# Kernel tuning notes

Measured on AMD Instinct MI355X. Metric: run time of the kernel, lower is better.

Reference implementation:

```python
import jax, jax.numpy as jnp
import numpy as np

B, N = 8192, 128          # batch, num intruders
D_OWN, D_GRID, D_INTR = 16, 512, 20
H, OUT = 128, 4


def setup_inputs() -> dict:
    key = jax.random.key(0)
    ks = jax.random.split(key, 12)
    rn = lambda k, shape, s=1.0: jax.random.normal(k, shape, jnp.float32) * s
    return {
        "state0": rn(ks[0], (B, D_OWN)),
        "state1": rn(ks[1], (B, D_GRID)),
        "state2": rn(ks[2], (B, N, D_INTR)),
        "W_own": rn(ks[3], (D_OWN, H), 0.1), "b_own": jnp.zeros((H,), jnp.float32),
        "W_intr": rn(ks[4], (D_INTR, H), 0.1), "b_intr": jnp.zeros((H,), jnp.float32),
        "W_grid": rn(ks[5], (D_GRID, H), 0.05), "b_grid": jnp.zeros((H,), jnp.float32),
        "Wq": rn(ks[6], (H, H), 0.08),
        "Wk": rn(ks[7], (H, H), 0.08),
        "Wv": rn(ks[8], (H, H), 0.08),
        "W1": rn(ks[9], (3 * H, H), 0.05), "b1": jnp.zeros((H,), jnp.float32),
        "W2": rn(ks[10], (H, OUT), 0.1), "b2": jnp.zeros((OUT,), jnp.float32),
    }


def reference(state0, state1, state2, W_own, b_own, W_intr, b_intr,
              W_grid, b_grid, Wq, Wk, Wv, W1, b1, W2, b2):
    own_e = jax.nn.relu(state0 @ W_own + b_own)            # [B,H]
    x_e = jax.nn.relu(state2 @ W_intr + b_intr)            # [B,N,H]
    q = own_e @ Wq                                         # [B,H]
    k = x_e @ Wk                                           # [B,N,H]
    v = x_e @ Wv                                           # [B,N,H]
    # mask = state2.mean(axis=2, keepdim=True).bool()  (nonzero test)
    mask = jnp.mean(state2, axis=2, keepdims=True) != 0    # [B,N,1]
    score = jnp.einsum('bnh,bh->bn', k, q)[..., None]      # bmm(k, q.unsqueeze(2)) -> [B,N,1]
    score = jnp.where(mask, score, -jnp.inf)
    alpha = jax.nn.softmax(score / np.float32(np.sqrt(H)), axis=1)
    alpha = jnp.where(mask, alpha, 0.0)
    v_att = jnp.sum(v * alpha, axis=1)                     # [B,H]
    own_grid = jax.nn.relu(state1 @ W_grid + b_grid)       # [B,H]
    concat = jnp.concatenate([own_e, v_att, own_grid], axis=1)  # [B,3H]
    out = (concat @ W1 + b1) @ W2 + b2                     # action_out_SAC
    mean = out
    log_std = jnp.clip(out, -20.0, 2.0)
    return mean, log_std
```

## Files before the change

### kernel.cpp

```cpp
#include <hip/hip_runtime.h>

typedef unsigned short ushort_t;
typedef __attribute__((ext_vector_type(8))) short bf16x8;
typedef __attribute__((ext_vector_type(4))) float f32x4;

__device__ __forceinline__ float bflo(unsigned u) { return __uint_as_float(u << 16); }
__device__ __forceinline__ float bfhi(unsigned u) { return __uint_as_float(u & 0xffff0000u); }
__device__ __forceinline__ float bfu(ushort_t s)  { return __uint_as_float((unsigned)s << 16); }
__device__ __forceinline__ ushort_t f2bf(float f) {
    unsigned u = __float_as_uint(f);
    u = u + 0x7fffu + ((u >> 16) & 1u);
    return (ushort_t)(u >> 16);
}
__device__ __forceinline__ void unpack8(uint4 v, float* f) {
    f[0]=bflo(v.x); f[1]=bfhi(v.x); f[2]=bflo(v.y); f[3]=bfhi(v.y);
    f[4]=bflo(v.z); f[5]=bfhi(v.z); f[6]=bflo(v.w); f[7]=bfhi(v.w);
}

__device__ __forceinline__ float load1(const void* p, size_t i, int f32) {
    return f32 ? ((const float*)p)[i] : bfu(((const ushort_t*)p)[i]);
}
__device__ __forceinline__ void load8(const void* p, size_t i, int f32, float* f) {
    if (f32) {
        const float4 a = *(const float4*)((const float*)p + i);
        const float4 b = *(const float4*)((const float*)p + i + 4);
        f[0]=a.x; f[1]=a.y; f[2]=a.z; f[3]=a.w;
        f[4]=b.x; f[5]=b.y; f[6]=b.z; f[7]=b.w;
    } else {
        unpack8(*(const uint4*)((const ushort_t*)p + i), f);
    }
}
__device__ __forceinline__ void load4(const void* p, size_t i, int f32, float* f) {
    if (f32) {
        const float4 a = *(const float4*)((const float*)p + i);
        f[0]=a.x; f[1]=a.y; f[2]=a.z; f[3]=a.w;
    } else {
        const uint2 u = *(const uint2*)((const ushort_t*)p + i);
        f[0]=bflo(u.x); f[1]=bfhi(u.x); f[2]=bflo(u.y); f[3]=bfhi(u.y);
    }
}

__device__ __forceinline__ int detect_f32(const ushort_t* s1h) {
    const int ln = threadIdx.x & 63;
    float v = fmaxf(fabsf(bfu(s1h[ln])), fabsf(bfu(s1h[ln + 64])));
    bool big = !(v <= 1e6f);
    return __ballot(big) != 0ull;
}

#define B_TOT 8192

__device__ __attribute__((aligned(16))) float    g_M[128 * 128];
__device__ __attribute__((aligned(16))) float    g_Wc1[384 * 4];
__device__ __attribute__((aligned(16))) float    g_Wv2[128 * 4];
__device__ __attribute__((aligned(16))) float    g_bc[4];
__device__ __attribute__((aligned(16))) float    g_t[B_TOT * 128];
__device__ __attribute__((aligned(16))) float    g_ogc[B_TOT * 4];
__device__ __attribute__((aligned(16))) ushort_t g_oe[B_TOT * 128];

__global__ __launch_bounds__(128) void k_pre(
    const void* __restrict__ Wq, const void* __restrict__ Wk,
    const void* __restrict__ Wv, const void* __restrict__ W1,
    const void* __restrict__ b1, const void* __restrict__ W2,
    const void* __restrict__ b2, const ushort_t* __restrict__ s1h)
{
    __shared__ float wq_sh[128];
    __shared__ float w2_sh[512];
    __shared__ float wc1_mid[512];
    __shared__ float redc[128][4];
    const int tid = threadIdx.x;
    const int bx = blockIdx.x;
    const int f32 = detect_f32(s1h);

    if (bx < 128) {
        wq_sh[tid] = load1(Wq, bx*128 + tid, f32);
        __syncthreads();
        float acc = 0.f;
        #pragma unroll
        for (int c = 0; c < 16; ++c) {
            float f[8]; load8(Wk, (size_t)tid*128 + c*8, f32, f);
            #pragma unroll
            for (int j = 0; j < 8; ++j) acc = fmaf(wq_sh[c*8+j], f[j], acc);
        }
        g_M[bx*128 + tid] = acc;
    } else {
        const int rbase = (bx == 128) ? 0 : ((bx == 129) ? 128 : 256);
        for (int i = tid; i < 512; i += 128) w2_sh[i] = load1(W2, i, f32);
        __syncthreads();

        const int r = rbase + tid;
        float a[4] = {0.f, 0.f, 0.f, 0.f};
        #pragma unroll
        for (int c = 0; c < 16; ++c) {
            float f[8]; load8(W1, (size_t)r*128 + c*8, f32, f);
            #pragma unroll
            for (int j = 0; j < 8; ++j) {
                const int p = c*8 + j;
                #pragma unroll
                for (int q = 0; q < 4; ++q) a[q] = fmaf(f[j], w2_sh[p*4+q], a[q]);
            }
        }
        #pragma unroll
        for (int q = 0; q < 4; ++q) g_Wc1[r*4+q] = a[q];

        if (bx == 129) {
            #pragma unroll
            for (int q = 0; q < 4; ++q) wc1_mid[tid*4+q] = a[q];
            __syncthreads();
            float v[4] = {0.f, 0.f, 0.f, 0.f};
            #pragma unroll
            for (int c = 0; c < 16; ++c) {
                float f[8]; load8(Wv, (size_t)tid*128 + c*8, f32, f);
                #pragma unroll
                for (int j = 0; j < 8; ++j) {
                    const int i2 = c*8 + j;
                    #pragma unroll
                    for (int q = 0; q < 4; ++q) v[q] = fmaf(f[j], wc1_mid[i2*4+q], v[q]);
                }
            }
            #pragma unroll
            for (int q = 0; q < 4; ++q) g_Wv2[tid*4+q] = v[q];

            const float bv = load1(b1, tid, f32);
            #pragma unroll
            for (int q = 0; q < 4; ++q) redc[tid][q] = bv * w2_sh[tid*4+q];
            __syncthreads();
            for (int s = 64; s > 0; s >>= 1) {
                if (tid < s) {
                    #pragma unroll
                    for (int q = 0; q < 4; ++q) redc[tid][q] += redc[tid+s][q];
                }
                __syncthreads();
            }
            if (tid < 4) g_bc[tid] = redc[0][tid] + load1(b2, tid, f32);
        }
    }
}

struct OwntSmem {
    float s0sh[16*16];
    float wosh[16*128];
    float bosh[128];
    float oesh[16*129];
    float Mt[32][128];
};
struct GridSmem {
    float s1T[32][18];
    float wg[32][128];
    float part[32][16][4];
};

__global__ __launch_bounds__(256) void k_og(
    const void* __restrict__ state0, const void* __restrict__ W_own,
    const void* __restrict__ b_own, const void* __restrict__ state1,
    const void* __restrict__ W_grid, const void* __restrict__ b_grid,
    const ushort_t* __restrict__ s1h)
{
    __shared__ __attribute__((aligned(16))) char smem_raw[
        sizeof(OwntSmem) > sizeof(GridSmem) ? sizeof(OwntSmem) : sizeof(GridSmem)];
    const int tid = threadIdx.x;
    const int bxx = blockIdx.x;
    const int f32 = detect_f32(s1h);

    if (bxx < 512) {
        OwntSmem& S = *reinterpret_cast<OwntSmem*>(smem_raw);
        const int b0 = bxx * 16;

        if (tid < 32) {
            float f[8]; load8(state0, (size_t)b0*16 + tid*8, f32, f);
            #pragma unroll
            for (int j = 0; j < 8; ++j) S.s0sh[tid*8 + j] = f[j];
        }
        {
            float f[8]; load8(W_own, (size_t)tid*8, f32, f);
            #pragma unroll
            for (int j = 0; j < 8; ++j) S.wosh[tid*8 + j] = f[j];
        }
        if (tid < 128) S.bosh[tid] = load1(b_own, tid, f32);
        __syncthreads();

        #pragma unroll
        for (int kk = 0; kk < 8; ++kk) {
            const int idx = tid + kk*256;
            const int bi = idx >> 7, h = idx & 127;
            float acc = S.bosh[h];
            #pragma unroll
            for (int d = 0; d < 16; ++d) acc = fmaf(S.s0sh[bi*16+d], S.wosh[d*128+h], acc);
            acc = fmaxf(acc, 0.f);
            S.oesh[bi*129 + h] = acc;
            g_oe[(size_t)(b0+bi)*128 + h] = f2bf(acc);
        }

        const int bi0 = (tid >> 5) * 2;
        const int h0  = (tid & 31) * 4;
        float t00=0.f,t01=0.f,t02=0.f,t03=0.f,t10=0.f,t11=0.f,t12=0.f,t13=0.f;
        for (int kt = 0; kt < 128; kt += 32) {
            __syncthreads();
            #pragma unroll
            for (int c = 0; c < 4; ++c) {
                const int i = tid + c*256;
                const int kk = i >> 5;
                const int hh = (i & 31) * 4;
                *(float4*)&S.Mt[kk][hh] = *(const float4*)&g_M[(size_t)(kt+kk)*128 + hh];
            }
            __syncthreads();
            #pragma unroll
            for (int k = 0; k < 32; ++k) {
                const float4 mv = *(const float4*)&S.Mt[k][h0];
                const float a0 = S.oesh[(bi0+0)*129 + kt + k];
                const float a1 = S.oesh[(bi0+1)*129 + kt + k];
                t00=fmaf(a0,mv.x,t00); t01=fmaf(a0,mv.y,t01); t02=fmaf(a0,mv.z,t02); t03=fmaf(a0,mv.w,t03);
                t10=fmaf(a1,mv.x,t10); t11=fmaf(a1,mv.y,t11); t12=fmaf(a1,mv.z,t12); t13=fmaf(a1,mv.w,t13);
            }
        }
        *(float4*)&g_t[(size_t)(b0+bi0+0)*128 + h0] = make_float4(t00,t01,t02,t03);
        *(float4*)&g_t[(size_t)(b0+bi0+1)*128 + h0] = make_float4(t10,t11,t12,t13);
    } else {
        GridSmem& S = *reinterpret_cast<GridSmem*>(smem_raw);
        const int b0 = (bxx - 512) * 16;

        const int bq = tid & 7;
        const int hq = tid >> 3;
        float a00=0.f,a01=0.f,a02=0.f,a03=0.f;
        float a10=0.f,a11=0.f,a12=0.f,a13=0.f;

        for (int kt = 0; kt < 512; kt += 32) {
            if (kt) __syncthreads();
            if (tid < 128) {
                const int bb = tid >> 3;
                const int kk = (tid & 7) * 4;
                float f[4];
                load4(state1, (size_t)(b0 + bb)*512 + kt + kk, f32, f);
                #pragma unroll
                for (int j = 0; j < 4; ++j) S.s1T[kk + j][bb] = f[j];
            }
            {
                #pragma unroll
                for (int c = 0; c < 4; ++c) {
                    const int i = tid + c*256;
                    const int kk = i >> 5;
                    const int hh = (i & 31) * 4;
                    float f[4];
                    load4(W_grid, (size_t)(kt + kk)*128 + hh, f32, f);
                    *(float4*)&S.wg[kk][hh] = make_float4(f[0], f[1], f[2], f[3]);
                }
            }
            __syncthreads();
            #pragma unroll 8
            for (int k = 0; k < 32; ++k) {
                const float x0 = S.s1T[k][bq*2 + 0];
                const float x1 = S.s1T[k][bq*2 + 1];
                const float4 w = *(const float4*)&S.wg[k][hq*4];
                a00=fmaf(x0,w.x,a00); a01=fmaf(x0,w.y,a01); a02=fmaf(x0,w.z,a02); a03=fmaf(x0,w.w,a03);
                a10=fmaf(x1,w.x,a10); a11=fmaf(x1,w.y,a11); a12=fmaf(x1,w.z,a12); a13=fmaf(x1,w.w,a13);
            }
        }

        float accs[2][4] = {{a00,a01,a02,a03},{a10,a11,a12,a13}};
        float pr[2][4] = {{0,0,0,0},{0,0,0,0}};
        #pragma unroll
        for (int jh = 0; jh < 4; ++jh) {
            const int h = hq*4 + jh;
            const float bg = load1(b_grid, h, f32);
            const float4 wc = *(const float4*)&g_Wc1[(256 + h)*4];
            #pragma unroll
            for (int ib = 0; ib < 2; ++ib) {
                const float og = fmaxf(accs[ib][jh] + bg, 0.f);
                pr[ib][0] = fmaf(og, wc.x, pr[ib][0]);
                pr[ib][1] = fmaf(og, wc.y, pr[ib][1]);
                pr[ib][2] = fmaf(og, wc.z, pr[ib][2]);
                pr[ib][3] = fmaf(og, wc.w, pr[ib][3]);
            }
        }
        __syncthreads();
        #pragma unroll
        for (int j = 0; j < 4; ++j) {
            S.part[hq][bq*2+0][j] = pr[0][j];
            S.part[hq][bq*2+1][j] = pr[1][j];
        }
        __syncthreads();
        if (tid < 64) {
            const int bb = tid >> 2, j = tid & 3;
            float s = 0.f;
            #pragma unroll
            for (int q = 0; q < 32; ++q) s += S.part[q][bb][j];
            g_ogc[(size_t)(b0 + bb)*4 + j] = s;
        }
    }
}

__global__ __launch_bounds__(256) void k_main(
    const void* __restrict__ state2, const void* __restrict__ W_intr,
    const void* __restrict__ b_intr, const ushort_t* __restrict__ s1h,
    void* __restrict__ out_raw)
{
    __shared__ __attribute__((aligned(16))) ushort_t wib[128 * 40];
    const int tid = threadIdx.x;
    const int f32 = detect_f32(s1h);

    #pragma unroll
    for (int c = 0; c < 10; ++c) {
        const int idx = c*256 + tid;
        const int d = idx >> 7, h = idx & 127;
        wib[h*40 + d] = f32 ? f2bf(((const float*)W_intr)[idx])
                            : ((const ushort_t*)W_intr)[idx];
    }
    if (tid < 128) {
        #pragma unroll
        for (int k = 20; k < 32; ++k) wib[tid*40 + k] = 0;
    }
    __syncthreads();

    const int wv = tid >> 6, ln = tid & 63, lq = ln >> 4, lc = ln & 15;
    const int b = blockIdx.x * 4 + wv;

    float bi_r[8], t_r[8];
    #pragma unroll
    for (int th = 0; th < 8; ++th) {
        bi_r[th] = load1(b_intr, th*16 + lc, f32);
        t_r[th]  = g_t[(size_t)b*128 + th*16 + lc] * 0.08838834764831845f;
    }

    bf16x8 A[8];
    unsigned msk[8];
    if (!f32) {
        const ushort_t* s2 = (const ushort_t*)state2;
        #pragma unroll
        for (int i = 0; i < 8; ++i) {
            const size_t rb = ((size_t)b*128 + i*16 + lc)*20 + lq*8;
            uint2 p0 = make_uint2(0u, 0u), p1 = make_uint2(0u, 0u);
            if (lq < 2)       { p0 = *(const uint2*)(s2 + rb); p1 = *(const uint2*)(s2 + rb + 4); }
            else if (lq == 2) { p0 = *(const uint2*)(s2 + rb); }
            union { bf16x8 v; uint2 u[2]; } cv;
            cv.u[0] = p0; cv.u[1] = p1;
            A[i] = cv.v;
            float s = bflo(p0.x)+bfhi(p0.x)+bflo(p0.y)+bfhi(p0.y)
                    + bflo(p1.x)+bfhi(p1.x)+bflo(p1.y)+bfhi(p1.y);
            s += __shfl_xor(s, 16);
            s += __shfl_xor(s, 32);
            msk[i] = (unsigned)(__ballot(s != 0.f) & 0xffffull);
        }
    } else {
        const float* s2 = (const float*)state2;
        #pragma unroll
        for (int i = 0; i < 8; ++i) {
            const size_t rb = ((size_t)b*128 + i*16 + lc)*20 + lq*8;
            float f[8] = {0.f,0.f,0.f,0.f,0.f,0.f,0.f,0.f};
            if (lq < 2) {
                const float4 a4 = *(const float4*)(s2 + rb);
                const float4 b4 = *(const float4*)(s2 + rb + 4);
                f[0]=a4.x; f[1]=a4.y; f[2]=a4.z; f[3]=a4.w;
                f[4]=b4.x; f[5]=b4.y; f[6]=b4.z; f[7]=b4.w;
            } else if (lq == 2) {
                const float4 a4 = *(const float4*)(s2 + rb);
                f[0]=a4.x; f[1]=a4.y; f[2]=a4.z; f[3]=a4.w;
            }
            union { bf16x8 v; ushort_t h[8]; } cv;
            float s = 0.f;
            #pragma unroll
            for (int j = 0; j < 8; ++j) { cv.h[j] = f2bf(f[j]); s += f[j]; }
            A[i] = cv.v;
            s += __shfl_xor(s, 16);
            s += __shfl_xor(s, 32);
            msk[i] = (unsigned)(__ballot(s != 0.f) & 0xffffull);
        }
    }

    const f32x4 zf = {0.f, 0.f, 0.f, 0.f};

    float sc[8][4];
    #pragma unroll
    for (int i = 0; i < 8; ++i)
        #pragma unroll
        for (int r = 0; r < 4; ++r) sc[i][r] = 0.f;

    #pragma unroll
    for (int th = 0; th < 8; ++th) {
        const bf16x8 Bv = *(const bf16x8*)&wib[(th*16 + lc)*40 + lq*8];
        #pragma unroll
        for (int i = 0; i < 8; ++i) {
            const f32x4 acc = __builtin_amdgcn_mfma_f32_16x16x32_bf16(A[i], Bv, zf, 0, 0, 0);
            #pragma unroll
            for (int r = 0; r < 4; ++r)
                sc[i][r] = fmaf(fmaxf(acc[r] + bi_r[th], 0.f), t_r[th], sc[i][r]);
        }
    }
    #pragma unroll
    for (int off = 1; off < 16; off <<= 1)
        #pragma unroll
        for (int i = 0; i < 8; ++i)
            #pragma unroll
            for (int r = 0; r < 4; ++r)
                sc[i][r] += __shfl_xor(sc[i][r], off);

    float m = -1e30f;
    #pragma unroll
    for (int i = 0; i < 8; ++i)
        #pragma unroll
        for (int r = 0; r < 4; ++r)
            if ((msk[i] >> (lq*4 + r)) & 1) m = fmaxf(m, sc[i][r]);
    m = fmaxf(m, __shfl_xor(m, 16));
    m = fmaxf(m, __shfl_xor(m, 32));

    float den = 0.f;
    #pragma unroll
    for (int i = 0; i < 8; ++i)
        #pragma unroll
        for (int r = 0; r < 4; ++r) {
            float e = 0.f;
            if ((msk[i] >> (lq*4 + r)) & 1) e = __expf(fmaxf(sc[i][r] - m, -80.f));
            sc[i][r] = e;
            den += e;
        }
    den += __shfl_xor(den, 16);
    den += __shfl_xor(den, 32);
    const float rden = (den > 0.f) ? (1.f / den) : 0.f;
    #pragma unroll
    for (int i = 0; i < 8; ++i)
        #pragma unroll
        for (int r = 0; r < 4; ++r) sc[i][r] *= rden;

    float o4[4] = {0.f, 0.f, 0.f, 0.f};
    #pragma unroll
    for (int th = 0; th < 8; ++th) {
        const bf16x8 Bv = *(const bf16x8*)&wib[(th*16 + lc)*40 + lq*8];
        float up = 0.f;
        #pragma unroll
        for (int i = 0; i < 8; ++i) {
            const f32x4 acc = __builtin_amdgcn_mfma_f32_16x16x32_bf16(A[i], Bv, zf, 0, 0, 0);
            #pragma unroll
            for (int r = 0; r < 4; ++r)
                up = fmaf(sc[i][r], fmaxf(acc[r] + bi_r[th], 0.f), up);
        }
        const float4 w2 = *(const float4*)&g_Wv2[(th*16 + lc)*4];
        o4[0] = fmaf(up, w2.x, o4[0]);
        o4[1] = fmaf(up, w2.y, o4[1]);
        o4[2] = fmaf(up, w2.z, o4[2]);
        o4[3] = fmaf(up, w2.w, o4[3]);
    }

    {
        const float oe0 = bfu(g_oe[(size_t)b*128 + ln]);
        const float oe1 = bfu(g_oe[(size_t)b*128 + 64 + ln]);
        const float4 wA = *(const float4*)&g_Wc1[ln*4];
        const float4 wB = *(const float4*)&g_Wc1[(64 + ln)*4];
        o4[0] += oe0*wA.x + oe1*wB.x;
        o4[1] += oe0*wA.y + oe1*wB.y;
        o4[2] += oe0*wA.z + oe1*wB.z;
        o4[3] += oe0*wA.w + oe1*wB.w;
    }

    #pragma unroll
    for (int off = 1; off < 64; off <<= 1)
        #pragma unroll
        for (int q = 0; q < 4; ++q)
            o4[q] += __shfl_xor(o4[q], off);

    if (ln == 0) {
        const float4 og = *(const float4*)&g_ogc[(size_t)b*4];
        const float v0 = g_bc[0] + og.x + o4[0];
        const float v1 = g_bc[1] + og.y + o4[1];
        const float v2 = g_bc[2] + og.z + o4[2];
        const float v3 = g_bc[3] + og.w + o4[3];
        const float l0 = fminf(fmaxf(v0, -20.f), 2.f);
        const float l1 = fminf(fmaxf(v1, -20.f), 2.f);
        const float l2 = fminf(fmaxf(v2, -20.f), 2.f);
        const float l3 = fminf(fmaxf(v3, -20.f), 2.f);
        if (f32) {
            float* of = (float*)out_raw;
            *(float4*)&of[(size_t)b*4] = make_float4(v0, v1, v2, v3);
            *(float4*)&of[((size_t)B_TOT + b)*4] = make_float4(l0, l1, l2, l3);
        } else {
            ushort_t* os = (ushort_t*)out_raw;
            uint2 mw, lw;
            mw.x = (unsigned)f2bf(v0) | ((unsigned)f2bf(v1) << 16);
            mw.y = (unsigned)f2bf(v2) | ((unsigned)f2bf(v3) << 16);
            lw.x = (unsigned)f2bf(l0) | ((unsigned)f2bf(l1) << 16);
            lw.y = (unsigned)f2bf(l2) | ((unsigned)f2bf(l3) << 16);
            *(uint2*)&os[(size_t)b*4] = mw;
            *(uint2*)&os[((size_t)B_TOT + b)*4] = lw;
        }
    }
}

extern "C" void kernel_launch(void* const* d_in, const int* in_sizes, int n_in,
                              void* d_out, int out_size, void* d_ws, size_t ws_size,
                              hipStream_t stream)
{
    (void)in_sizes; (void)n_in; (void)out_size; (void)d_ws; (void)ws_size;
    const void* state0 = d_in[0];
    const void* state1 = d_in[1];
    const void* state2 = d_in[2];
    const void* W_own  = d_in[3];
    const void* b_own  = d_in[4];
    const void* W_intr = d_in[5];
    const void* b_intr = d_in[6];
    const void* W_grid = d_in[7];
    const void* b_grid = d_in[8];
    const void* Wq     = d_in[9];
    const void* Wk     = d_in[10];
    const void* Wv     = d_in[11];
    const void* W1     = d_in[12];
    const void* b1     = d_in[13];
    const void* W2     = d_in[14];
    const void* b2     = d_in[15];
    const ushort_t* s1h = (const ushort_t*)state1;

    k_pre  <<<dim3(131),  dim3(128), 0, stream>>>(Wq, Wk, Wv, W1, b1, W2, b2, s1h);
    k_og   <<<dim3(1024), dim3(256), 0, stream>>>(state0, W_own, b_own, state1, W_grid, b_grid, s1h);
    k_main <<<dim3(2048), dim3(256), 0, stream>>>(state2, W_intr, b_intr, s1h, d_out);
}
```

Baseline: 282.9 us.

## Merge weight-precompute kernel into own/grid kernel, recomputing Wq·Wk per block

Removes the separate k_pre launch by folding its work into the own/grid kernel. Own-path blocks now compute q = own_e·Wq and then q·Wk^T directly instead of reading a precomputed g_M. Grid blocks recompute their slice of W1·W2 locally in shared memory, and two extra blocks produce the remaining g_Wc1, g_Wv2 and g_bc. This saves one launch and the serial dependency between the first two kernels. In exchange every block does redundant weight arithmetic and reads Wk/W1 from global memory.

```diff
diff --git a/kernel.cpp b/kernel.cpp
--- a/kernel.cpp
+++ b/kernel.cpp
@@ -49,7 +49,6 @@
 
 #define B_TOT 8192
 
-__device__ __attribute__((aligned(16))) float    g_M[128 * 128];
 __device__ __attribute__((aligned(16))) float    g_Wc1[384 * 4];
 __device__ __attribute__((aligned(16))) float    g_Wv2[128 * 4];
 __device__ __attribute__((aligned(16))) float    g_bc[4];
@@ -57,106 +56,31 @@
 __device__ __attribute__((aligned(16))) float    g_ogc[B_TOT * 4];
 __device__ __attribute__((aligned(16))) ushort_t g_oe[B_TOT * 128];
 
-__global__ __launch_bounds__(128) void k_pre(
-    const void* __restrict__ Wq, const void* __restrict__ Wk,
-    const void* __restrict__ Wv, const void* __restrict__ W1,
-    const void* __restrict__ b1, const void* __restrict__ W2,
-    const void* __restrict__ b2, const ushort_t* __restrict__ s1h)
-{
-    __shared__ float wq_sh[128];
-    __shared__ float w2_sh[512];
-    __shared__ float wc1_mid[512];
-    __shared__ float redc[128][4];
-    const int tid = threadIdx.x;
-    const int bx = blockIdx.x;
-    const int f32 = detect_f32(s1h);
-
-    if (bx < 128) {
-        wq_sh[tid] = load1(Wq, bx*128 + tid, f32);
-        __syncthreads();
-        float acc = 0.f;
-        #pragma unroll
-        for (int c = 0; c < 16; ++c) {
-            float f[8]; load8(Wk, (size_t)tid*128 + c*8, f32, f);
-            #pragma unroll
-            for (int j = 0; j < 8; ++j) acc = fmaf(wq_sh[c*8+j], f[j], acc);
-        }
-        g_M[bx*128 + tid] = acc;
-    } else {
-        const int rbase = (bx == 128) ? 0 : ((bx == 129) ? 128 : 256);
-        for (int i = tid; i < 512; i += 128) w2_sh[i] = load1(W2, i, f32);
-        __syncthreads();
-
-        const int r = rbase + tid;
-        float a[4] = {0.f, 0.f, 0.f, 0.f};
-        #pragma unroll
-        for (int c = 0; c < 16; ++c) {
-            float f[8]; load8(W1, (size_t)r*128 + c*8, f32, f);
-            #pragma unroll
-            for (int j = 0; j < 8; ++j) {
-                const int p = c*8 + j;
-                #pragma unroll
-                for (int q = 0; q < 4; ++q) a[q] = fmaf(f[j], w2_sh[p*4+q], a[q]);
-            }
-        }
-        #pragma unroll
-        for (int q = 0; q < 4; ++q) g_Wc1[r*4+q] = a[q];
-
-        if (bx == 129) {
-            #pragma unroll
-            for (int q = 0; q < 4; ++q) wc1_mid[tid*4+q] = a[q];
-            __syncthreads();
-            float v[4] = {0.f, 0.f, 0.f, 0.f};
-            #pragma unroll
-            for (int c = 0; c < 16; ++c) {
-                float f[8]; load8(Wv, (size_t)tid*128 + c*8, f32, f);
-                #pragma unroll
-                for (int j = 0; j < 8; ++j) {
-                    const int i2 = c*8 + j;
-                    #pragma unroll
-                    for (int q = 0; q < 4; ++q) v[q] = fmaf(f[j], wc1_mid[i2*4+q], v[q]);
-                }
-            }
-            #pragma unroll
-            for (int q = 0; q < 4; ++q) g_Wv2[tid*4+q] = v[q];
-
-            const float bv = load1(b1, tid, f32);
-            #pragma unroll
-            for (int q = 0; q < 4; ++q) redc[tid][q] = bv * w2_sh[tid*4+q];
-            __syncthreads();
-            for (int s = 64; s > 0; s >>= 1) {
-                if (tid < s) {
-                    #pragma unroll
-                    for (int q = 0; q < 4; ++q) redc[tid][q] += redc[tid+s][q];
-                }
-                __syncthreads();
-            }
-            if (tid < 4) g_bc[tid] = redc[0][tid] + load1(b2, tid, f32);
-        }
-    }
-}
-
+struct OwntA { float s0sh[256]; float wosh[2048]; float bosh[128]; };
 struct OwntSmem {
-    float s0sh[16*16];
-    float wosh[16*128];
-    float bosh[128];
-    float oesh[16*129];
+    union { OwntA a; float qT[128 * 18]; } u;
+    float oesh[16 * 129];
     float Mt[32][128];
 };
 struct GridSmem {
     float s1T[32][18];
     float wg[32][128];
     float part[32][16][4];
+    float w2s[512];
+    float wcsl[512];
 };
-
-__global__ __launch_bounds__(256) void k_og(
+struct PreSmem { float w2_sh[512]; float wc1_mid[512]; float redc[128][4]; };
+
+__global__ __launch_bounds__(256) void k_prep(
     const void* __restrict__ state0, const void* __restrict__ W_own,
     const void* __restrict__ b_own, const void* __restrict__ state1,
     const void* __restrict__ W_grid, const void* __restrict__ b_grid,
-    const ushort_t* __restrict__ s1h)
+    const void* __restrict__ Wq, const void* __restrict__ Wk,
+    const void* __restrict__ Wv, const void* __restrict__ W1,
+    const void* __restrict__ b1, const void* __restrict__ W2,
+    const void* __restrict__ b2, const ushort_t* __restrict__ s1h)
 {
-    __shared__ __attribute__((aligned(16))) char smem_raw[
-        sizeof(OwntSmem) > sizeof(GridSmem) ? sizeof(OwntSmem) : sizeof(GridSmem)];
+    __shared__ __attribute__((aligned(16))) char smem_raw[sizeof(OwntSmem)];
     const int tid = threadIdx.x;
     const int bxx = blockIdx.x;
     const int f32 = detect_f32(s1h);
@@ -168,23 +92,23 @@
         if (tid < 32) {
             float f[8]; load8(state0, (size_t)b0*16 + tid*8, f32, f);
             #pragma unroll
-            for (int j = 0; j < 8; ++j) S.s0sh[tid*8 + j] = f[j];
+            for (int j = 0; j < 8; ++j) S.u.a.s0sh[tid*8 + j] = f[j];
         }
         {
             float f[8]; load8(W_own, (size_t)tid*8, f32, f);
             #pragma unroll
-            for (int j = 0; j < 8; ++j) S.wosh[tid*8 + j] = f[j];
-        }
-        if (tid < 128) S.bosh[tid] = load1(b_own, tid, f32);
+            for (int j = 0; j < 8; ++j) S.u.a.wosh[tid*8 + j] = f[j];
+        }
+        if (tid < 128) S.u.a.bosh[tid] = load1(b_own, tid, f32);
         __syncthreads();
 
         #pragma unroll
         for (int kk = 0; kk < 8; ++kk) {
             const int idx = tid + kk*256;
             const int bi = idx >> 7, h = idx & 127;
-            float acc = S.bosh[h];
-            #pragma unroll
-            for (int d = 0; d < 16; ++d) acc = fmaf(S.s0sh[bi*16+d], S.wosh[d*128+h], acc);
+            float acc = S.u.a.bosh[h];
+            #pragma unroll
+            for (int d = 0; d < 16; ++d) acc = fmaf(S.u.a.s0sh[bi*16+d], S.u.a.wosh[d*128+h], acc);
             acc = fmaxf(acc, 0.f);
             S.oesh[bi*129 + h] = acc;
             g_oe[(size_t)(b0+bi)*128 + h] = f2bf(acc);
@@ -192,7 +116,7 @@
 
         const int bi0 = (tid >> 5) * 2;
         const int h0  = (tid & 31) * 4;
-        float t00=0.f,t01=0.f,t02=0.f,t03=0.f,t10=0.f,t11=0.f,t12=0.f,t13=0.f;
+        float q00=0.f,q01=0.f,q02=0.f,q03=0.f,q10=0.f,q11=0.f,q12=0.f,q13=0.f;
         for (int kt = 0; kt < 128; kt += 32) {
             __syncthreads();
             #pragma unroll
@@ -200,7 +124,9 @@
                 const int i = tid + c*256;
                 const int kk = i >> 5;
                 const int hh = (i & 31) * 4;
-                *(float4*)&S.Mt[kk][hh] = *(const float4*)&g_M[(size_t)(kt+kk)*128 + hh];
+                float f[4];
+                load4(Wq, (size_t)(kt+kk)*128 + hh, f32, f);
+                *(float4*)&S.Mt[kk][hh] = make_float4(f[0], f[1], f[2], f[3]);
             }
             __syncthreads();
             #pragma unroll
@@ -208,15 +134,63 @@
                 const float4 mv = *(const float4*)&S.Mt[k][h0];
                 const float a0 = S.oesh[(bi0+0)*129 + kt + k];
                 const float a1 = S.oesh[(bi0+1)*129 + kt + k];
-                t00=fmaf(a0,mv.x,t00); t01=fmaf(a0,mv.y,t01); t02=fmaf(a0,mv.z,t02); t03=fmaf(a0,mv.w,t03);
-                t10=fmaf(a1,mv.x,t10); t11=fmaf(a1,mv.y,t11); t12=fmaf(a1,mv.z,t12); t13=fmaf(a1,mv.w,t13);
-            }
-        }
-        *(float4*)&g_t[(size_t)(b0+bi0+0)*128 + h0] = make_float4(t00,t01,t02,t03);
-        *(float4*)&g_t[(size_t)(b0+bi0+1)*128 + h0] = make_float4(t10,t11,t12,t13);
-    } else {
+                q00=fmaf(a0,mv.x,q00); q01=fmaf(a0,mv.y,q01); q02=fmaf(a0,mv.z,q02); q03=fmaf(a0,mv.w,q03);
+                q10=fmaf(a1,mv.x,q10); q11=fmaf(a1,mv.y,q11); q12=fmaf(a1,mv.z,q12); q13=fmaf(a1,mv.w,q13);
+            }
+        }
+        {
+            const float qq[2][4] = {{q00,q01,q02,q03},{q10,q11,q12,q13}};
+            #pragma unroll
+            for (int i = 0; i < 4; ++i)
+                #pragma unroll
+                for (int ib = 0; ib < 2; ++ib)
+                    S.u.qT[(h0+i)*18 + (bi0+ib)] = qq[ib][i];
+        }
+        __syncthreads();
+
+        {
+            const int j  = tid >> 1;
+            const int b8 = (tid & 1) * 8;
+            float tacc[8] = {0.f,0.f,0.f,0.f,0.f,0.f,0.f,0.f};
+            #pragma unroll
+            for (int c = 0; c < 16; ++c) {
+                float wf[8]; load8(Wk, (size_t)j*128 + c*8, f32, wf);
+                #pragma unroll
+                for (int jj = 0; jj < 8; ++jj) {
+                    const int k = c*8 + jj;
+                    #pragma unroll
+                    for (int ib = 0; ib < 8; ++ib)
+                        tacc[ib] = fmaf(wf[jj], S.u.qT[k*18 + b8 + ib], tacc[ib]);
+                }
+            }
+            #pragma unroll
+            for (int ib = 0; ib < 8; ++ib)
+                g_t[(size_t)(b0 + b8 + ib)*128 + j] = tacc[ib];
+        }
+    } else if (bxx < 1024) {
         GridSmem& S = *reinterpret_cast<GridSmem*>(smem_raw);
         const int b0 = (bxx - 512) * 16;
+
+        for (int i = tid; i < 512; i += 256) S.w2s[i] = load1(W2, i, f32);
+        __syncthreads();
+        {
+            const int r  = tid >> 1;
+            const int jp = (tid & 1) * 2;
+            float acc0 = 0.f, acc1 = 0.f;
+            #pragma unroll
+            for (int c = 0; c < 16; ++c) {
+                float wf[8]; load8(W1, (size_t)(256 + r)*128 + c*8, f32, wf);
+                #pragma unroll
+                for (int jj = 0; jj < 8; ++jj) {
+                    const int mm = c*8 + jj;
+                    acc0 = fmaf(wf[jj], S.w2s[mm*4 + jp],     acc0);
+                    acc1 = fmaf(wf[jj], S.w2s[mm*4 + jp + 1], acc1);
+                }
+            }
+            S.wcsl[r*4 + jp]     = acc0;
+            S.wcsl[r*4 + jp + 1] = acc1;
+        }
+        __syncthreads();
 
         const int bq = tid & 7;
         const int hq = tid >> 3;
@@ -261,7 +235,7 @@
         for (int jh = 0; jh < 4; ++jh) {
             const int h = hq*4 + jh;
             const float bg = load1(b_grid, h, f32);
-            const float4 wc = *(const float4*)&g_Wc1[(256 + h)*4];
+            const float4 wc = *(const float4*)&S.wcsl[h*4];
             #pragma unroll
             for (int ib = 0; ib < 2; ++ib) {
                 const float og = fmaxf(accs[ib][jh] + bg, 0.f);
@@ -284,6 +258,59 @@
             #pragma unroll
             for (int q = 0; q < 32; ++q) s += S.part[q][bb][j];
             g_ogc[(size_t)(b0 + bb)*4 + j] = s;
+        }
+    } else {
+        PreSmem& S = *reinterpret_cast<PreSmem*>(smem_raw);
+        const int rbase = (bxx == 1024) ? 0 : 128;
+        for (int i = tid; i < 512; i += 256) S.w2_sh[i] = load1(W2, i, f32);
+        __syncthreads();
+
+        const int rt = tid & 127;
+        const int r = rbase + rt;
+        float a[4] = {0.f, 0.f, 0.f, 0.f};
+        #pragma unroll
+        for (int c = 0; c < 16; ++c) {
+            float f[8]; load8(W1, (size_t)r*128 + c*8, f32, f);
+            #pragma unroll
+            for (int j = 0; j < 8; ++j) {
+                const int p = c*8 + j;
+                #pragma unroll
+                for (int q = 0; q < 4; ++q) a[q] = fmaf(f[j], S.w2_sh[p*4+q], a[q]);
+            }
+        }
+        #pragma unroll
+        for (int q = 0; q < 4; ++q) g_Wc1[r*4+q] = a[q];
+
+        if (bxx == 1025) {
+            #pragma unroll
+            for (int q = 0; q < 4; ++q) S.wc1_mid[rt*4+q] = a[q];
+            __syncthreads();
+            float v[4] = {0.f, 0.f, 0.f, 0.f};
+            #pragma unroll
+            for (int c = 0; c < 16; ++c) {
+                float f[8]; load8(Wv, (size_t)rt*128 + c*8, f32, f);
+                #pragma unroll
+                for (int j = 0; j < 8; ++j) {
+                    const int i2 = c*8 + j;
+                    #pragma unroll
+                    for (int q = 0; q < 4; ++q) v[q] = fmaf(f[j], S.wc1_mid[i2*4+q], v[q]);
+                }
+            }
+            #pragma unroll
+            for (int q = 0; q < 4; ++q) g_Wv2[rt*4+q] = v[q];
+
+            const float bv = load1(b1, rt, f32);
+            #pragma unroll
+            for (int q = 0; q < 4; ++q) S.redc[rt][q] = bv * S.w2_sh[rt*4+q];
+            __syncthreads();
+            for (int s = 64; s > 0; s >>= 1) {
+                if (tid < s) {
+                    #pragma unroll
+                    for (int q = 0; q < 4; ++q) S.redc[tid][q] += S.redc[tid+s][q];
+                }
+                __syncthreads();
+            }
+            if (tid < 4) g_bc[tid] = S.redc[0][tid] + load1(b2, tid, f32);
         }
     }
 }
@@ -505,7 +532,8 @@
     const void* b2     = d_in[15];
     const ushort_t* s1h = (const ushort_t*)state1;
 
-    k_pre  <<<dim3(131),  dim3(128), 0, stream>>>(Wq, Wk, Wv, W1, b1, W2, b2, s1h);
-    k_og   <<<dim3(1024), dim3(256), 0, stream>>>(state0, W_own, b_own, state1, W_grid, b_grid, s1h);
+    k_prep <<<dim3(1026), dim3(256), 0, stream>>>(state0, W_own, b_own,
+                                                  state1, W_grid, b_grid,
+                                                  Wq, Wk, Wv, W1, b1, W2, b2, s1h);
     k_main <<<dim3(2048), dim3(256), 0, stream>>>(state2, W_intr, b_intr, s1h, d_out);
 }
```

Measured after the change: 465.2 us. 64.5% more time.
